# Kernel tuning notes

Hardware: AMD Instinct MI355X
Metric: run time of the kernel (lower is better)

The kernel has to match this reference:

```python
import jax, jax.numpy as jnp
import numpy as np

# dims
B, NB, T, NC = 16, 55, 512, 8          # batch, filter bands, time steps, CSP comps
D, L, H, E, K, F, C = 512, 6, 8, 8, 2, 2048, 2  # embed, depth, heads, experts, top_k, d_ff, classes
DH = D // H
IN = NB * NC  # 440
EPS = 1e-5


def _ln(x, s, b):
    m = x.mean(-1, keepdims=True)
    v = ((x - m) ** 2).mean(-1, keepdims=True)
    return (x - m) / jnp.sqrt(v + EPS) * s + b


def setup_inputs() -> dict:
    key = jax.random.key(0)
    ks = iter(jax.random.split(key, 64))
    n = lambda shape, s=0.02: jax.random.normal(next(ks), shape, jnp.float32) * s
    inp = {
        "x": jax.random.normal(next(ks), (B, NB, T, NC), jnp.float32),
        # frontend
        "proj_w": n((IN, D)), "proj_b": jnp.zeros((D,), jnp.float32),
        "pos": n((1, T, D)),
        "ln_pre_s": jnp.ones((D,), jnp.float32), "ln_pre_b": jnp.zeros((D,), jnp.float32),
        # stacked transformer-block params [L, ...]
        "ln1_s": jnp.ones((L, D), jnp.float32), "ln1_b": jnp.zeros((L, D), jnp.float32),
        "wq": n((L, D, D)), "bq": jnp.zeros((L, D), jnp.float32),
        "wk": n((L, D, D)), "bk": jnp.zeros((L, D), jnp.float32),
        "wv": n((L, D, D)), "bv": jnp.zeros((L, D), jnp.float32),
        "wo": n((L, D, D)), "bo": jnp.zeros((L, D), jnp.float32),
        "ln2_s": jnp.ones((L, D), jnp.float32), "ln2_b": jnp.zeros((L, D), jnp.float32),
        "gate_w": n((L, D, E)),
        "e_w1": n((L, E, D, F)), "e_b1": jnp.zeros((L, E, F), jnp.float32),
        "e_w2": n((L, E, F, D)), "e_b2": jnp.zeros((L, E, D), jnp.float32),
        # classifier head
        "ln_f_s": jnp.ones((D,), jnp.float32), "ln_f_b": jnp.zeros((D,), jnp.float32),
        "head_w": n((D, C)), "head_b": jnp.zeros((C,), jnp.float32),
    }
    return inp


def _moe(h, gw, w1, b1, w2, b2):
    # h: [N, D]; top-K softmax-gated mixture of GELU-FFN experts + load-balance aux loss
    N = h.shape[0]
    probs = jax.nn.softmax(h @ gw, axis=-1)                  # [N, E]
    vals, idx = jax.lax.top_k(probs, K)                      # [N, K]
    w = vals / vals.sum(-1, keepdims=True)                   # renormalized top-k weights
    disp = jax.nn.one_hot(idx, E, dtype=h.dtype)             # [N, K, E]
    combine = (disp * w[..., None]).sum(1)                   # [N, E]
    y = jnp.zeros_like(h)
    for e in range(E):  # small fixed expert loop
        y = y + combine[:, e:e + 1] * (jax.nn.gelu(h @ w1[e] + b1[e]) @ w2[e] + b2[e])
    frac = disp.mean((0, 1)) * K                             # fraction of tokens routed to each expert
    aux = E * jnp.sum(frac * probs.mean(0))
    return y, aux


def reference(x, proj_w, proj_b, pos, ln_pre_s, ln_pre_b, ln1_s, ln1_b, wq, bq, wk, bk,
              wv, bv, wo, bo, ln2_s, ln2_b, gate_w, e_w1, e_b1, e_w2, e_b2,
              ln_f_s, ln_f_b, head_w, head_b):
    b, nb, t, nc = x.shape
    h = x.transpose(0, 2, 1, 3).reshape(b, t, nb * nc) @ proj_w + proj_b  # [B,T,D]
    h = _ln(h + pos[:, :t, :], ln_pre_s, ln_pre_b)
    scale = DH ** -0.5
    total_aux = jnp.float32(0.0)
    for l in range(L):
        # pre-LN multi-head self-attention
        a = _ln(h, ln1_s[l], ln1_b[l])
        q = (a @ wq[l] + bq[l]).reshape(b, t, H, DH)
        k = (a @ wk[l] + bk[l]).reshape(b, t, H, DH)
        v = (a @ wv[l] + bv[l]).reshape(b, t, H, DH)
        att = jax.nn.softmax(jnp.einsum('bqhd,bkhd->bhqk', q, k) * scale, axis=-1)
        o = jnp.einsum('bhqk,bkhd->bqhd', att, v).reshape(b, t, D) @ wo[l] + bo[l]
        h = h + o
        # pre-LN MoE FFN
        m = _ln(h, ln2_s[l], ln2_b[l]).reshape(b * t, D)
        y, aux = _moe(m, gate_w[l], e_w1[l], e_b1[l], e_w2[l], e_b2[l])
        h = h + y.reshape(b, t, D)
        total_aux = total_aux + aux
    pooled = h.mean(axis=1)                                   # [B, D]
    logits = _ln(pooled, ln_f_s, ln_f_b) @ head_w + head_b    # [B, C]
    return logits, total_aux
```

## Files before the change

### kernel.cpp

```cpp
#include <hip/hip_runtime.h>
#include <stdint.h>

typedef unsigned short u16;
typedef unsigned int   u32;
typedef short bh8 __attribute__((ext_vector_type(8)));
typedef float f4  __attribute__((ext_vector_type(4)));

#define NTOK    8192
#define PADROWS 17408
#define MAXTILES 136

__device__ __forceinline__ u16 f2bf(float f){
  u32 u = __float_as_uint(f);
  return (u16)((u + 0x7fffu + ((u>>16)&1u)) >> 16);
}
__device__ __forceinline__ float bf2f(u16 h){ return __uint_as_float(((u32)h)<<16); }
__device__ __forceinline__ u32 pk2(float a, float b){ return (u32)f2bf(a) | ((u32)f2bf(b)<<16); }
__device__ __forceinline__ float gelu_f(float x){
  float u = 0.7978845608028654f*(x + 0.044715f*x*x*x);
  float t = 1.f - 2.f/(__expf(2.f*u)+1.f);
  return 0.5f*x*(1.f+t);
}
__device__ __forceinline__ void gload_lds16(const void* g, void* l){
  __builtin_amdgcn_global_load_lds((const __attribute__((address_space(1))) u32*)g,
                                   (__attribute__((address_space(3))) u32*)l, 16, 0, 0);
}

__global__ __launch_bounds__(256) void xpose_k(const float* __restrict__ x, u16* __restrict__ xt){
  int idx = blockIdx.x*256 + threadIdx.x;
  const float* src = x + (size_t)idx*8;
  float4 a = *(const float4*)src;
  float4 b = *(const float4*)(src+4);
  int t  = idx & 511;
  int nb = (idx>>9) % 55;
  int bb = (idx>>9) / 55;
  uint4 u;
  u.x = pk2(a.x,a.y); u.y = pk2(a.z,a.w); u.z = pk2(b.x,b.y); u.w = pk2(b.z,b.w);
  *(uint4*)&xt[((size_t)(bb*512+t))*448 + nb*8] = u;
}

__device__ __forceinline__ void tile_xpose(const float* __restrict__ src, u16* __restrict__ dst,
                                           int Ksrc, int N, int Kdst, float (*tile)[65])
{
  int tid = threadIdx.x;
  int k0 = blockIdx.y*64, n0 = blockIdx.x*64;
  #pragma unroll
  for (int p=0;p<4;++p){
    int r = p*16 + (tid>>4);
    int c4 = (tid&15)*4;
    int k = k0 + r;
    float4 v = (k < Ksrc) ? *(const float4*)&src[(size_t)k*N + n0 + c4] : (float4){0.f,0.f,0.f,0.f};
    tile[r][c4]=v.x; tile[r][c4+1]=v.y; tile[r][c4+2]=v.z; tile[r][c4+3]=v.w;
  }
  __syncthreads();
  #pragma unroll
  for (int p=0;p<2;++p){
    int rn = p*32 + (tid>>3);
    int ck = (tid&7)*8;
    uint4 u;
    u.x = pk2(tile[ck+0][rn], tile[ck+1][rn]);
    u.y = pk2(tile[ck+2][rn], tile[ck+3][rn]);
    u.z = pk2(tile[ck+4][rn], tile[ck+5][rn]);
    u.w = pk2(tile[ck+6][rn], tile[ck+7][rn]);
    *(uint4*)&dst[(size_t)(n0+rn)*Kdst + k0 + ck] = u;
  }
}

__global__ __launch_bounds__(256) void wconv_k(const float* __restrict__ src, u16* __restrict__ dst,
                                               int Ksrc, int N, int Kdst){
  __shared__ float tile[64][65];
  src += (size_t)blockIdx.z*Ksrc*N;
  dst += (size_t)blockIdx.z*N*Kdst;
  tile_xpose(src, dst, Ksrc, N, Kdst, tile);
}

__global__ __launch_bounds__(256) void wconvqkvo_k(const float* __restrict__ wq, const float* __restrict__ wk,
    const float* __restrict__ wv, const float* __restrict__ wo,
    u16* __restrict__ qkvt, u16* __restrict__ wot)
{
  __shared__ float tile[64][65];
  int z = blockIdx.z;
  int l = z>>2, which = z&3;
  const float* src = ((which==0)? wq : (which==1)? wk : (which==2)? wv : wo) + (size_t)l*512*512;
  u16* dst = (which==3) ? wot + (size_t)l*512*512
                        : qkvt + (size_t)l*1536*512 + (size_t)which*512*512;
  tile_xpose(src, dst, 512, 512, 512, tile);
}

__global__ __launch_bounds__(256) void qkvb_k(const float* __restrict__ bq, const float* __restrict__ bk,
                                              const float* __restrict__ bv, float* __restrict__ qkvb){
  int idx = blockIdx.x*256 + threadIdx.x;
  int l = idx/1536, c = idx - l*1536;
  const float* s = (c<512)? bq : (c<1024)? bk : bv;
  qkvb[idx] = s[l*512 + (c&511)];
}

template<int MODE, bool GATHER>
__global__ __launch_bounds__(256) void gemm2_k(
    const u16* __restrict__ A, int lda,
    const u16* __restrict__ Bt, int ldb, int Ksteps,
    const float* __restrict__ biasBase,
    float* __restrict__ Cf, u16* __restrict__ Cb, int ldc,
    const int* __restrict__ tile_e, const int* __restrict__ toklist,
    const float* __restrict__ wlist, int expN)
{
  __shared__ __align__(16) u16 As[2][128*32];
  __shared__ __align__(16) u16 Bs[2][128*32];
  const int tid = threadIdx.x, lane = tid&63, w = tid>>6;
  const int wr = w>>1, wc = w&1;
  int nx = gridDim.x;
  int nwg = nx * gridDim.y;
  int lin = blockIdx.y*nx + blockIdx.x;
  int qq = nwg>>3, rr = nwg&7, xc = lin&7, oo = lin>>3;
  int wg = (xc<rr ? xc*(qq+1) : rr*(qq+1)+(xc-rr)*qq) + oo;
  int by = wg/nx, bx = wg - by*nx;
  const int n0 = bx*128, m0 = by*128;
  const u16* Bp = Bt;
  const float* bias = biasBase;
  if constexpr (MODE>=3){
    int e = tile_e[by];
    Bp   += (size_t)e*(size_t)expN*(size_t)ldb;
    bias += (size_t)e*(size_t)expN;
  }
  const u16* asrc0; const u16* asrc1; const u16* bsrc0; const u16* bsrc1;
  {
    int idx0 = tid, row0 = idx0>>2, sp0 = idx0&3, ks0 = sp0 ^ ((row0>>1)&3);
    int idx1 = 256+tid, row1 = idx1>>2, sp1 = idx1&3, ks1 = sp1 ^ ((row1>>1)&3);
    size_t ar0 = GATHER ? (size_t)toklist[m0+row0] : (size_t)(m0+row0);
    size_t ar1 = GATHER ? (size_t)toklist[m0+row1] : (size_t)(m0+row1);
    asrc0 = A + ar0*(size_t)lda + ks0*8;
    asrc1 = A + ar1*(size_t)lda + ks1*8;
    bsrc0 = Bp + (size_t)(n0+row0)*ldb + ks0*8;
    bsrc1 = Bp + (size_t)(n0+row1)*ldb + ks1*8;
  }
  f4 acc[4][4];
  #pragma unroll
  for (int i=0;i<4;++i)
    #pragma unroll
    for (int j=0;j<4;++j) acc[i][j] = (f4){0.f,0.f,0.f,0.f};

  gload_lds16(asrc0, &As[0][tid*8]);
  gload_lds16(asrc1, &As[0][(256+tid)*8]);
  gload_lds16(bsrc0, &Bs[0][tid*8]);
  gload_lds16(bsrc1, &Bs[0][(256+tid)*8]);
  asrc0 += 32; asrc1 += 32; bsrc0 += 32; bsrc1 += 32;
  __syncthreads();

  int buf = 0;
  for (int kt=0; kt<Ksteps; ++kt){
    if (kt+1 < Ksteps){
      int nb = buf^1;
      gload_lds16(asrc0, &As[nb][tid*8]);
      gload_lds16(asrc1, &As[nb][(256+tid)*8]);
      gload_lds16(bsrc0, &Bs[nb][tid*8]);
      gload_lds16(bsrc1, &Bs[nb][(256+tid)*8]);
      asrc0 += 32; asrc1 += 32; bsrc0 += 32; bsrc1 += 32;
    }
    bh8 af[4], bf[4];
    const int q = lane>>4;
    #pragma unroll
    for (int mf=0;mf<4;++mf){
      int r = wr*64 + mf*16 + (lane&15);
      af[mf] = *(const bh8*)&As[buf][r*32 + (q ^ ((r>>1)&3))*8];
    }
    #pragma unroll
    for (int nf=0;nf<4;++nf){
      int r = wc*64 + nf*16 + (lane&15);
      bf[nf] = *(const bh8*)&Bs[buf][r*32 + (q ^ ((r>>1)&3))*8];
    }
    #pragma unroll
    for (int mf=0;mf<4;++mf)
      #pragma unroll
      for (int nf=0;nf<4;++nf)
        acc[mf][nf] = __builtin_amdgcn_mfma_f32_16x16x32_bf16(af[mf], bf[nf], acc[mf][nf], 0, 0, 0);
    __syncthreads();
    buf ^= 1;
  }
  #pragma unroll
  for (int mf=0;mf<4;++mf){
    #pragma unroll
    for (int nf=0;nf<4;++nf){
      f4 d = acc[mf][nf];
      int ncol = n0 + wc*64 + nf*16 + (lane&15);
      float bv = bias[ncol];
      #pragma unroll
      for (int r=0;r<4;++r){
        int mrow = m0 + wr*64 + mf*16 + (lane>>4)*4 + r;
        float val = d[r] + bv;
        if constexpr (MODE==0){
          Cf[(size_t)mrow*ldc + ncol] = val;
        } else if constexpr (MODE==1){
          int slab = ncol>>6, dh = ncol&63;
          Cb[((size_t)slab*NTOK + (size_t)mrow)*64 + dh] = f2bf(val);
        } else if constexpr (MODE==2){
          Cf[(size_t)mrow*ldc + ncol] += val;
        } else if constexpr (MODE==3){
          Cb[(size_t)mrow*ldc + ncol] = f2bf(gelu_f(val));
        } else {
          Cb[(size_t)mrow*ldc + ncol] = f2bf(wlist[mrow]*val);
        }
      }
    }
  }
}

template<bool ADDPOS, bool OUTF32>
__global__ __launch_bounds__(256) void ln_k(const float* __restrict__ X, const float* __restrict__ pos,
    const float* __restrict__ sc, const float* __restrict__ bi,
    float* __restrict__ outF, u16* __restrict__ outB)
{
  int tid=threadIdx.x, lane=tid&63, w=tid>>6;
  int row = blockIdx.x*4 + w;
  const float* xr = X + (size_t)row*512 + lane*8;
  float x[8];
  float4 v0 = *(const float4*)xr;
  float4 v1 = *(const float4*)(xr+4);
  x[0]=v0.x;x[1]=v0.y;x[2]=v0.z;x[3]=v0.w;x[4]=v1.x;x[5]=v1.y;x[6]=v1.z;x[7]=v1.w;
  if constexpr (ADDPOS){
    const float* pr = pos + (size_t)(row&511)*512 + lane*8;
    float4 p0 = *(const float4*)pr, p1 = *(const float4*)(pr+4);
    x[0]+=p0.x;x[1]+=p0.y;x[2]+=p0.z;x[3]+=p0.w;x[4]+=p1.x;x[5]+=p1.y;x[6]+=p1.z;x[7]+=p1.w;
  }
  float sm=0.f, sq=0.f;
  #pragma unroll
  for (int i=0;i<8;++i){ sm+=x[i]; sq+=x[i]*x[i]; }
  #pragma unroll
  for (int mk=1; mk<64; mk<<=1){ sm += __shfl_xor(sm, mk); sq += __shfl_xor(sq, mk); }
  float mean = sm*(1.f/512.f);
  float var  = sq*(1.f/512.f) - mean*mean;
  float rstd = rsqrtf(var + 1e-5f);
  int d0 = lane*8;
  float4 s0 = *(const float4*)(sc+d0), s1 = *(const float4*)(sc+d0+4);
  float4 b0 = *(const float4*)(bi+d0), b1 = *(const float4*)(bi+d0+4);
  float y[8];
  y[0]=(x[0]-mean)*rstd*s0.x+b0.x; y[1]=(x[1]-mean)*rstd*s0.y+b0.y;
  y[2]=(x[2]-mean)*rstd*s0.z+b0.z; y[3]=(x[3]-mean)*rstd*s0.w+b0.w;
  y[4]=(x[4]-mean)*rstd*s1.x+b1.x; y[5]=(x[5]-mean)*rstd*s1.y+b1.y;
  y[6]=(x[6]-mean)*rstd*s1.z+b1.z; y[7]=(x[7]-mean)*rstd*s1.w+b1.w;
  if constexpr (OUTF32){
    float4 o0 = {y[0],y[1],y[2],y[3]}, o1 = {y[4],y[5],y[6],y[7]};
    *(float4*)(outF + (size_t)row*512 + d0)     = o0;
    *(float4*)(outF + (size_t)row*512 + d0 + 4) = o1;
  } else {
    uint4 u; u.x=pk2(y[0],y[1]); u.y=pk2(y[2],y[3]); u.z=pk2(y[4],y[5]); u.w=pk2(y[6],y[7]);
    *(uint4*)&outB[(size_t)row*512 + d0] = u;
  }
}

__global__ __launch_bounds__(256) void gatherln_k(float* __restrict__ h,
    const u16* __restrict__ yb, const int* __restrict__ t2pos,
    const float* __restrict__ sc, const float* __restrict__ bi, u16* __restrict__ outB)
{
  int tid=threadIdx.x, lane=tid&63, w=tid>>6;
  int row = blockIdx.x*4 + w;
  float* hp = h + (size_t)row*512 + lane*8;
  float4 v0 = *(float4*)hp, v1 = *(float4*)(hp+4);
  int p0 = t2pos[2*row], p1 = t2pos[2*row+1];
  uint4 ya = *(const uint4*)&yb[(size_t)p0*512 + lane*8];
  uint4 yv = *(const uint4*)&yb[(size_t)p1*512 + lane*8];
  float x[8];
  x[0]=v0.x + bf2f((u16)(ya.x&0xffff)) + bf2f((u16)(yv.x&0xffff));
  x[1]=v0.y + bf2f((u16)(ya.x>>16))    + bf2f((u16)(yv.x>>16));
  x[2]=v0.z + bf2f((u16)(ya.y&0xffff)) + bf2f((u16)(yv.y&0xffff));
  x[3]=v0.w + bf2f((u16)(ya.y>>16))    + bf2f((u16)(yv.y>>16));
  x[4]=v1.x + bf2f((u16)(ya.z&0xffff)) + bf2f((u16)(yv.z&0xffff));
  x[5]=v1.y + bf2f((u16)(ya.z>>16))    + bf2f((u16)(yv.z>>16));
  x[6]=v1.z + bf2f((u16)(ya.w&0xffff)) + bf2f((u16)(yv.w&0xffff));
  x[7]=v1.w + bf2f((u16)(ya.w>>16))    + bf2f((u16)(yv.w>>16));
  float4 o0 = {x[0],x[1],x[2],x[3]}, o1 = {x[4],x[5],x[6],x[7]};
  *(float4*)hp = o0; *(float4*)(hp+4) = o1;
  float sm=0.f, sq=0.f;
  #pragma unroll
  for (int i=0;i<8;++i){ sm+=x[i]; sq+=x[i]*x[i]; }
  #pragma unroll
  for (int mk=1; mk<64; mk<<=1){ sm += __shfl_xor(sm, mk); sq += __shfl_xor(sq, mk); }
  float mean = sm*(1.f/512.f);
  float rstd = rsqrtf(sq*(1.f/512.f) - mean*mean + 1e-5f);
  int d0 = lane*8;
  float4 s0 = *(const float4*)(sc+d0), s1 = *(const float4*)(sc+d0+4);
  float4 b0 = *(const float4*)(bi+d0), b1 = *(const float4*)(bi+d0+4);
  float y[8];
  y[0]=(x[0]-mean)*rstd*s0.x+b0.x; y[1]=(x[1]-mean)*rstd*s0.y+b0.y;
  y[2]=(x[2]-mean)*rstd*s0.z+b0.z; y[3]=(x[3]-mean)*rstd*s0.w+b0.w;
  y[4]=(x[4]-mean)*rstd*s1.x+b1.x; y[5]=(x[5]-mean)*rstd*s1.y+b1.y;
  y[6]=(x[6]-mean)*rstd*s1.z+b1.z; y[7]=(x[7]-mean)*rstd*s1.w+b1.w;
  uint4 u; u.x=pk2(y[0],y[1]); u.y=pk2(y[2],y[3]); u.z=pk2(y[4],y[5]); u.w=pk2(y[6],y[7]);
  *(uint4*)&outB[(size_t)row*512 + d0] = u;
}

__global__ __launch_bounds__(256) void attn_k(const u16* __restrict__ QKV, u16* __restrict__ Og)
{
  __shared__ __align__(16) u16 VT[2][64*72];
  __shared__ __align__(16) u16 PS[4][16*72];
  int tid=threadIdx.x, lane=tid&63, w=tid>>6;
  int qt=blockIdx.x, hh=blockIdx.y, bb=blockIdx.z;
  const u16* Qh = QKV + ((size_t)hh     *NTOK + (size_t)bb*512)*64;
  const u16* Kh = QKV + ((size_t)(8+hh) *NTOK + (size_t)bb*512)*64;
  const u16* Vh = QKV + ((size_t)(16+hh)*NTOK + (size_t)bb*512)*64;
  size_t obase = (size_t)bb*512*512 + (size_t)hh*64;
  int qrow0 = qt*64 + w*16;
  bh8 qf[2];
  #pragma unroll
  for (int kf=0;kf<2;++kf)
    qf[kf] = *(const bh8*)&Qh[ (size_t)(qrow0 + (lane&15))*64 + kf*32 + (lane>>4)*8 ];
  f4 oacc[4];
  #pragma unroll
  for (int i=0;i<4;++i) oacc[i] = (f4){0.f,0.f,0.f,0.f};
  float mrun[4] = {-1e30f,-1e30f,-1e30f,-1e30f};
  float lrun[4] = {0.f,0.f,0.f,0.f};
  const float scale = 0.125f;

  for (int kt=0; kt<8; ++kt){
    const int buf = kt&1;
    #pragma unroll
    for (int r2=0;r2<2;++r2){
      int idx = r2*256 + tid;
      int dhg = idx&7;
      int dh0 = dhg*8, key = idx>>3;
      uint4 raw = *(const uint4*)&Vh[ (size_t)(kt*64+key)*64 + dh0 ];
      int kx = key ^ (dhg<<3);
      u32 rw[4] = {raw.x, raw.y, raw.z, raw.w};
      #pragma unroll
      for (int j=0;j<4;++j){
        VT[buf][(dh0+2*j  )*72 + kx] = (u16)(rw[j]&0xffff);
        VT[buf][(dh0+2*j+1)*72 + kx] = (u16)(rw[j]>>16);
      }
    }
    f4 s[4];
    #pragma unroll
    for (int nf=0;nf<4;++nf){
      size_t krow = (size_t)(kt*64+nf*16+(lane&15))*64 + (lane>>4)*8;
      bh8 k0 = *(const bh8*)&Kh[krow];
      bh8 k1 = *(const bh8*)&Kh[krow+32];
      f4 z = (f4){0.f,0.f,0.f,0.f};
      z = __builtin_amdgcn_mfma_f32_16x16x32_bf16(qf[0], k0, z, 0,0,0);
      z = __builtin_amdgcn_mfma_f32_16x16x32_bf16(qf[1], k1, z, 0,0,0);
      s[nf] = z;
    }
    float pe[4][4];
    #pragma unroll
    for (int r=0;r<4;++r){
      float sv0=s[0][r]*scale, sv1=s[1][r]*scale, sv2=s[2][r]*scale, sv3=s[3][r]*scale;
      float mt = fmaxf(fmaxf(sv0,sv1), fmaxf(sv2,sv3));
      #pragma unroll
      for (int mk=1; mk<16; mk<<=1) mt = fmaxf(mt, __shfl_xor(mt, mk));
      float mn = fmaxf(mrun[r], mt);
      float sf = __expf(mrun[r]-mn);
      float p0=__expf(sv0-mn), p1=__expf(sv1-mn), p2=__expf(sv2-mn), p3=__expf(sv3-mn);
      pe[0][r]=p0; pe[1][r]=p1; pe[2][r]=p2; pe[3][r]=p3;
      float rs = p0+p1+p2+p3;
      #pragma unroll
      for (int mk=1; mk<16; mk<<=1) rs += __shfl_xor(rs, mk);
      lrun[r] = lrun[r]*sf + rs;
      mrun[r] = mn;
      #pragma unroll
      for (int df=0;df<4;++df) oacc[df][r] *= sf;
    }
    #pragma unroll
    for (int nf=0;nf<4;++nf)
      #pragma unroll
      for (int r=0;r<4;++r)
        PS[w][ ((lane>>4)*4+r)*72 + nf*16 + (lane&15) ] = f2bf(pe[nf][r]);
    __syncthreads();
    #pragma unroll
    for (int ks=0;ks<2;++ks){
      bh8 pa = *(const bh8*)&PS[w][ (lane&15)*72 + ks*32 + (lane>>4)*8 ];
      #pragma unroll
      for (int df=0;df<4;++df){
        int dh = df*16 + (lane&15);
        int sgrp = (dh>>3)&7;
        bh8 vb = *(const bh8*)&VT[buf][ dh*72 + ((ks*4 + (lane>>4)) ^ sgrp)*8 ];
        oacc[df] = __builtin_amdgcn_mfma_f32_16x16x32_bf16(pa, vb, oacc[df], 0,0,0);
      }
    }
  }
  #pragma unroll
  for (int df=0;df<4;++df)
    #pragma unroll
    for (int r=0;r<4;++r){
      int qr = qrow0 + (lane>>4)*4 + r;
      float ov = oacc[df][r] / lrun[r];
      Og[ obase + (size_t)qr*512 + df*16 + (lane&15) ] = f2bf(ov);
    }
}

__global__ __launch_bounds__(256) void lnroute_k(const float* __restrict__ h,
    const float* __restrict__ sc, const float* __restrict__ bi, u16* __restrict__ outB,
    const float* __restrict__ gw,
    float* __restrict__ psum, int* __restrict__ cnt, int* __restrict__ t2e, float* __restrict__ t2w)
{
  __shared__ float ps[8]; __shared__ int cs[8];
  int tid=threadIdx.x, lane=tid&63, w=tid>>6;
  if (tid<8){ ps[tid]=0.f; cs[tid]=0; }
  __syncthreads();
  int d0 = lane*8;
  float4 s0 = *(const float4*)(sc+d0), s1 = *(const float4*)(sc+d0+4);
  float4 b0 = *(const float4*)(bi+d0), b1 = *(const float4*)(bi+d0+4);
  for (int it=0; it<4; ++it){
    int t = blockIdx.x*16 + w*4 + it;
    const float* xr = h + (size_t)t*512 + d0;
    float x[8];
    float4 v0 = *(const float4*)xr, v1 = *(const float4*)(xr+4);
    x[0]=v0.x;x[1]=v0.y;x[2]=v0.z;x[3]=v0.w;x[4]=v1.x;x[5]=v1.y;x[6]=v1.z;x[7]=v1.w;
    float sm=0.f, sq=0.f;
    #pragma unroll
    for (int i=0;i<8;++i){ sm+=x[i]; sq+=x[i]*x[i]; }
    #pragma unroll
    for (int mk=1; mk<64; mk<<=1){ sm += __shfl_xor(sm, mk); sq += __shfl_xor(sq, mk); }
    float mean = sm*(1.f/512.f);
    float rstd = rsqrtf(sq*(1.f/512.f) - mean*mean + 1e-5f);
    float y[8];
    y[0]=(x[0]-mean)*rstd*s0.x+b0.x; y[1]=(x[1]-mean)*rstd*s0.y+b0.y;
    y[2]=(x[2]-mean)*rstd*s0.z+b0.z; y[3]=(x[3]-mean)*rstd*s0.w+b0.w;
    y[4]=(x[4]-mean)*rstd*s1.x+b1.x; y[5]=(x[5]-mean)*rstd*s1.y+b1.y;
    y[6]=(x[6]-mean)*rstd*s1.z+b1.z; y[7]=(x[7]-mean)*rstd*s1.w+b1.w;
    uint4 u; u.x=pk2(y[0],y[1]); u.y=pk2(y[2],y[3]); u.z=pk2(y[4],y[5]); u.w=pk2(y[6],y[7]);
    *(uint4*)&outB[(size_t)t*512 + d0] = u;
    float acc[8] = {0,0,0,0,0,0,0,0};
    #pragma unroll
    for (int j=0;j<8;++j){
      const float* g = gw + (size_t)(d0+j)*8;
      float4 g0 = *(const float4*)g, g1 = *(const float4*)(g+4);
      acc[0]+=y[j]*g0.x; acc[1]+=y[j]*g0.y; acc[2]+=y[j]*g0.z; acc[3]+=y[j]*g0.w;
      acc[4]+=y[j]*g1.x; acc[5]+=y[j]*g1.y; acc[6]+=y[j]*g1.z; acc[7]+=y[j]*g1.w;
    }
    #pragma unroll
    for (int mk=1; mk<64; mk<<=1)
      #pragma unroll
      for (int e=0;e<8;++e) acc[e] += __shfl_xor(acc[e], mk);
    if (lane==0){
      float mx=acc[0];
      #pragma unroll
      for (int e=1;e<8;++e) mx = fmaxf(mx, acc[e]);
      float pe[8], tot=0.f;
      #pragma unroll
      for (int e=0;e<8;++e){ pe[e]=__expf(acc[e]-mx); tot+=pe[e]; }
      float inv = 1.f/tot;
      #pragma unroll
      for (int e=0;e<8;++e) pe[e]*=inv;
      int e0=0; float v0=pe[0];
      #pragma unroll
      for (int e=1;e<8;++e) if (pe[e]>v0){ v0=pe[e]; e0=e; }
      int e1=-1; float v1=-1.f;
      #pragma unroll
      for (int e=0;e<8;++e) if (e!=e0 && pe[e]>v1){ v1=pe[e]; e1=e; }
      float invw = 1.f/(v0+v1);
      t2e[2*t]=e0; t2w[2*t]=v0*invw; t2e[2*t+1]=e1; t2w[2*t+1]=v1*invw;
      #pragma unroll
      for (int e=0;e<8;++e) atomicAdd(&ps[e], pe[e]);
      atomicAdd(&cs[e0],1); atomicAdd(&cs[e1],1);
    }
  }
  __syncthreads();
  if (tid<8){ atomicAdd(&psum[tid], ps[tid]); atomicAdd(&cnt[tid], cs[tid]); }
}

__global__ __launch_bounds__(256) void offsets_k(const int* __restrict__ cnt, const float* __restrict__ psum,
    int* __restrict__ offs, int* __restrict__ fill, int* __restrict__ tile_e,
    int* __restrict__ toklist, float* __restrict__ wlist, float* __restrict__ auxp)
{
  int tid = threadIdx.x, b = blockIdx.x;
  int i = b*256 + tid;
  if (i < PADROWS){ toklist[i]=0; wlist[i]=0.f; }
  if (b==0){
    if (tid==0){
      int off=0; float auxl=0.f;
      for (int e=0;e<8;++e){
        offs[e] = off;
        int reg = (cnt[e]+127)&~127;
        int t0 = off>>7, t1 = (off+reg)>>7;
        for (int t=t0;t<t1;++t) tile_e[t]=e;
        off += reg;
        auxl += ((float)cnt[e]*(1.f/8192.f)) * (psum[e]*(1.f/8192.f));
      }
      for (int t=off>>7; t<MAXTILES; ++t) tile_e[t]=0;
      auxp[0] += 8.f*auxl;
    }
    if (tid<8) fill[tid]=0;
  }
}

__global__ __launch_bounds__(256) void scatter_k(const int* __restrict__ t2e, const float* __restrict__ t2w,
    const int* __restrict__ offs, int* __restrict__ fill,
    int* __restrict__ toklist, float* __restrict__ wlist, int* __restrict__ t2pos)
{
  int t = blockIdx.x*256 + threadIdx.x;
  #pragma unroll
  for (int kk=0;kk<2;++kk){
    int e = t2e[2*t+kk];
    int p = atomicAdd(&fill[e], 1);
    int i = offs[e] + p;
    toklist[i] = t; wlist[i] = t2w[2*t+kk]; t2pos[2*t+kk] = i;
  }
}

__global__ __launch_bounds__(256) void gather_k(float* __restrict__ h, const u16* __restrict__ yb,
                                                const int* __restrict__ t2pos)
{
  int tid = threadIdx.x;
  int t = blockIdx.x*4 + (tid>>6);
  int lane = tid&63;
  int p0 = t2pos[2*t], p1 = t2pos[2*t+1];
  uint4 a = *(const uint4*)&yb[(size_t)p0*512 + lane*8];
  uint4 b = *(const uint4*)&yb[(size_t)p1*512 + lane*8];
  float* hp = h + (size_t)t*512 + lane*8;
  float4 h0 = *(float4*)hp, h1 = *(float4*)(hp+4);
  h0.x += bf2f((u16)(a.x&0xffff)) + bf2f((u16)(b.x&0xffff));
  h0.y += bf2f((u16)(a.x>>16))    + bf2f((u16)(b.x>>16));
  h0.z += bf2f((u16)(a.y&0xffff)) + bf2f((u16)(b.y&0xffff));
  h0.w += bf2f((u16)(a.y>>16))    + bf2f((u16)(b.y>>16));
  h1.x += bf2f((u16)(a.z&0xffff)) + bf2f((u16)(b.z&0xffff));
  h1.y += bf2f((u16)(a.z>>16))    + bf2f((u16)(b.z>>16));
  h1.z += bf2f((u16)(a.w&0xffff)) + bf2f((u16)(b.w&0xffff));
  h1.w += bf2f((u16)(a.w>>16))    + bf2f((u16)(b.w>>16));
  *(float4*)hp = h0; *(float4*)(hp+4) = h1;
}

__global__ __launch_bounds__(256) void pool_k(const float* __restrict__ h, float* __restrict__ pooled){
  int idx = blockIdx.x*256 + threadIdx.x;
  int bb = idx>>9, d = idx&511;
  const float* p = h + (size_t)bb*512*512 + d;
  float s=0.f;
  for (int t=0;t<512;++t) s += p[(size_t)t*512];
  pooled[idx] = s*(1.f/512.f);
}

__global__ __launch_bounds__(256) void head_k(const float* __restrict__ pooled,
    const float* __restrict__ sc, const float* __restrict__ bi,
    const float* __restrict__ hw, const float* __restrict__ hb,
    const float* __restrict__ auxp, float* __restrict__ out)
{
  int tid=threadIdx.x, lane=tid&63, w=tid>>6;
  for (int i=0;i<4;++i){
    int row = w*4+i;
    const float* xr = pooled + (size_t)row*512 + lane*8;
    float x[8];
    float4 v0 = *(const float4*)xr, v1 = *(const float4*)(xr+4);
    x[0]=v0.x;x[1]=v0.y;x[2]=v0.z;x[3]=v0.w;x[4]=v1.x;x[5]=v1.y;x[6]=v1.z;x[7]=v1.w;
    float sm=0.f, sq=0.f;
    #pragma unroll
    for (int j=0;j<8;++j){ sm+=x[j]; sq+=x[j]*x[j]; }
    #pragma unroll
    for (int mk=1; mk<64; mk<<=1){ sm += __shfl_xor(sm, mk); sq += __shfl_xor(sq, mk); }
    float mean = sm*(1.f/512.f);
    float rstd = rsqrtf(sq*(1.f/512.f) - mean*mean + 1e-5f);
    int d0 = lane*8;
    float c0=0.f, c1=0.f;
    #pragma unroll
    for (int j=0;j<8;++j){
      float yv = (x[j]-mean)*rstd*sc[d0+j] + bi[d0+j];
      c0 += yv*hw[(d0+j)*2]; c1 += yv*hw[(d0+j)*2+1];
    }
    #pragma unroll
    for (int mk=1; mk<64; mk<<=1){ c0 += __shfl_xor(c0, mk); c1 += __shfl_xor(c1, mk); }
    if (lane==0){ out[row*2+0] = c0 + hb[0]; out[row*2+1] = c1 + hb[1]; }
  }
  if (tid==0) out[32] = auxp[0];
}

extern "C" void kernel_launch(void* const* d_in, const int* in_sizes, int n_in,
                              void* d_out, int out_size, void* d_ws, size_t ws_size,
                              hipStream_t stream)
{
  (void)in_sizes; (void)n_in; (void)out_size; (void)ws_size;
  const float* x      = (const float*)d_in[0];
  const float* proj_w = (const float*)d_in[1];
  const float* proj_b = (const float*)d_in[2];
  const float* pos    = (const float*)d_in[3];
  const float* ln_pre_s=(const float*)d_in[4];
  const float* ln_pre_b=(const float*)d_in[5];
  const float* ln1_s  = (const float*)d_in[6];
  const float* ln1_b  = (const float*)d_in[7];
  const float* wq     = (const float*)d_in[8];
  const float* bq     = (const float*)d_in[9];
  const float* wk     = (const float*)d_in[10];
  const float* bk     = (const float*)d_in[11];
  const float* wv     = (const float*)d_in[12];
  const float* bv     = (const float*)d_in[13];
  const float* wo     = (const float*)d_in[14];
  const float* bo     = (const float*)d_in[15];
  const float* ln2_s  = (const float*)d_in[16];
  const float* ln2_b  = (const float*)d_in[17];
  const float* gate_w = (const float*)d_in[18];
  const float* e_w1   = (const float*)d_in[19];
  const float* e_b1   = (const float*)d_in[20];
  const float* e_w2   = (const float*)d_in[21];
  const float* e_b2   = (const float*)d_in[22];
  const float* ln_f_s = (const float*)d_in[23];
  const float* ln_f_b = (const float*)d_in[24];
  const float* head_w = (const float*)d_in[25];
  const float* head_b = (const float*)d_in[26];

  char* base = (char*)d_ws;
  size_t off = 0;
  auto carve = [&](size_t bytes)->char*{
    char* r = base + off; off += (bytes + 255) & ~(size_t)255; return r;
  };
  u16*   xt      = (u16*)  carve((size_t)8192*448*2);
  float* h       = (float*)carve((size_t)8192*512*4);
  u16*   a       = (u16*)  carve((size_t)8192*512*2);
  u16*   qkv     = (u16*)  carve((size_t)8192*1536*2);
  u16*   ob      = (u16*)  carve((size_t)8192*512*2);
  u16*   hidden  = (u16*)  carve((size_t)PADROWS*2048*2);
  u16*   ybuf    = (u16*)  carve((size_t)PADROWS*512*2);
  u16*   projt   = (u16*)  carve((size_t)512*448*2);
  u16*   qkvt    = (u16*)  carve((size_t)6*1536*512*2);
  u16*   wot     = (u16*)  carve((size_t)6*512*512*2);
  u16*   w1t     = (u16*)  carve((size_t)6*8*2048*512*2);
  u16*   w2t     = (u16*)  carve((size_t)6*8*512*2048*2);
  float* qkvb    = (float*)carve((size_t)6*1536*4);
  int*   toklist = (int*)  carve(PADROWS*4);
  float* wlist   = (float*)carve(PADROWS*4);
  int*   tile_e  = (int*)  carve(256*4);
  int*   rcntA   = (int*)  carve(6*16*4);
  int*   fill    = (int*)  carve(64);
  int*   offs    = (int*)  carve(64);
  int*   t2e     = (int*)  carve(16384*4);
  float* t2w     = (float*)carve(16384*4);
  int*   t2pos   = (int*)  carve(16384*4);
  float* pooled  = (float*)carve(8192*4);
  float* auxp    = (float*)carve(256);

  hipMemsetAsync(xt, 0, (size_t)8192*448*2, stream);
  hipMemsetAsync(rcntA, 0, 6*16*4, stream);
  hipMemsetAsync(auxp, 0, 4, stream);

  xpose_k<<<1760, 256, 0, stream>>>(x, xt);
  wconv_k<<<dim3(8,7,1), 256, 0, stream>>>(proj_w, projt, 440, 512, 448);
  wconvqkvo_k<<<dim3(8,8,24), 256, 0, stream>>>(wq, wk, wv, wo, qkvt, wot);
  wconv_k<<<dim3(32,8,48), 256, 0, stream>>>(e_w1, w1t, 512, 2048, 512);
  wconv_k<<<dim3(8,32,48), 256, 0, stream>>>(e_w2, w2t, 2048, 512, 2048);
  qkvb_k<<<36, 256, 0, stream>>>(bq, bk, bv, qkvb);
  gemm2_k<0,false><<<dim3(4,64), 256, 0, stream>>>(xt, 448, projt, 448, 14, proj_b,
      h, nullptr, 512, nullptr, nullptr, nullptr, 0);
  ln_k<true,true><<<2048, 256, 0, stream>>>(h, pos, ln_pre_s, ln_pre_b, h, nullptr);

  for (int l=0; l<6; ++l){
    int*   cnt  = rcntA + l*16;
    float* psum = (float*)(cnt + 8);
    if (l == 0)
      ln_k<false,false><<<2048, 256, 0, stream>>>(h, nullptr, ln1_s, ln1_b, nullptr, a);
    else
      gatherln_k<<<2048, 256, 0, stream>>>(h, ybuf, t2pos,
          ln1_s+(size_t)l*512, ln1_b+(size_t)l*512, a);
    gemm2_k<1,false><<<dim3(12,64), 256, 0, stream>>>(a, 512, qkvt+(size_t)l*1536*512, 512, 16,
        qkvb+(size_t)l*1536, nullptr, qkv, 1536, nullptr, nullptr, nullptr, 0);
    attn_k<<<dim3(8,8,16), 256, 0, stream>>>(qkv, ob);
    gemm2_k<2,false><<<dim3(4,64), 256, 0, stream>>>(ob, 512, wot+(size_t)l*512*512, 512, 16,
        bo+(size_t)l*512, h, nullptr, 512, nullptr, nullptr, nullptr, 0);
    lnroute_k<<<512, 256, 0, stream>>>(h, ln2_s+(size_t)l*512, ln2_b+(size_t)l*512, a,
        gate_w+(size_t)l*512*8, psum, cnt, t2e, t2w);
    offsets_k<<<68, 256, 0, stream>>>(cnt, psum, offs, fill, tile_e, toklist, wlist, auxp);
    scatter_k<<<32, 256, 0, stream>>>(t2e, t2w, offs, fill, toklist, wlist, t2pos);
    gemm2_k<3,true ><<<dim3(16,MAXTILES), 256, 0, stream>>>(a, 512, w1t+(size_t)l*8*2048*512, 512, 16,
        e_b1 + (size_t)l*8*2048, nullptr, hidden, 2048, tile_e, toklist, wlist, 2048);
    gemm2_k<4,false><<<dim3(4,MAXTILES), 256, 0, stream>>>(hidden, 2048, w2t+(size_t)l*8*512*2048, 2048, 64,
        e_b2 + (size_t)l*8*512, nullptr, ybuf, 512, tile_e, nullptr, wlist, 512);
  }

  gather_k<<<2048, 256, 0, stream>>>(h, ybuf, t2pos);
  pool_k<<<32, 256, 0, stream>>>(h, pooled);
  head_k<<<1, 256, 0, stream>>>(pooled, ln_f_s, ln_f_b, head_w, head_b, auxp, (float*)d_out);
}
```

Before: 2.322 ms.

## Store V transposed in QKV GEMM epilogue and read it directly in attention

The QKV projection epilogue now writes the V slabs in a dh-major (transposed) layout as packed bf16 pairs, while Q and K keep the old layout. The attention kernel drops its per-tile LDS transpose of V and the block-wide barrier, and loads the MFMA B-operand fragments for V straight from global memory. This removes the LDS shuffle and the synchronisation from the attention loop. In exchange the GEMM epilogue does strided scattered stores, and attention relies on cache hits for repeated V reads.

```diff
diff --git a/kernel.cpp b/kernel.cpp
--- a/kernel.cpp
+++ b/kernel.cpp
@@ -183,21 +183,33 @@
       f4 d = acc[mf][nf];
       int ncol = n0 + wc*64 + nf*16 + (lane&15);
       float bv = bias[ncol];
-      #pragma unroll
-      for (int r=0;r<4;++r){
-        int mrow = m0 + wr*64 + mf*16 + (lane>>4)*4 + r;
-        float val = d[r] + bv;
-        if constexpr (MODE==0){
-          Cf[(size_t)mrow*ldc + ncol] = val;
-        } else if constexpr (MODE==1){
-          int slab = ncol>>6, dh = ncol&63;
-          Cb[((size_t)slab*NTOK + (size_t)mrow)*64 + dh] = f2bf(val);
-        } else if constexpr (MODE==2){
-          Cf[(size_t)mrow*ldc + ncol] += val;
-        } else if constexpr (MODE==3){
-          Cb[(size_t)mrow*ldc + ncol] = f2bf(gelu_f(val));
+      int mrow0 = m0 + wr*64 + mf*16 + (lane>>4)*4;
+      if constexpr (MODE==1){
+        int slab = ncol>>6, dh = ncol&63;
+        if (slab < 16){
+          #pragma unroll
+          for (int r=0;r<4;++r)
+            Cb[((size_t)slab*NTOK + (size_t)(mrow0+r))*64 + dh] = f2bf(d[r]+bv);
         } else {
-          Cb[(size_t)mrow*ldc + ncol] = f2bf(wlist[mrow]*val);
+          uint2 u;
+          u.x = pk2(d[0]+bv, d[1]+bv);
+          u.y = pk2(d[2]+bv, d[3]+bv);
+          *(uint2*)&Cb[(size_t)slab*NTOK*64 + (size_t)dh*NTOK + mrow0] = u;
+        }
+      } else {
+        #pragma unroll
+        for (int r=0;r<4;++r){
+          int mrow = mrow0 + r;
+          float val = d[r] + bv;
+          if constexpr (MODE==0){
+            Cf[(size_t)mrow*ldc + ncol] = val;
+          } else if constexpr (MODE==2){
+            Cf[(size_t)mrow*ldc + ncol] += val;
+          } else if constexpr (MODE==3){
+            Cb[(size_t)mrow*ldc + ncol] = f2bf(gelu_f(val));
+          } else {
+            Cb[(size_t)mrow*ldc + ncol] = f2bf(wlist[mrow]*val);
+          }
         }
       }
     }
@@ -290,13 +302,12 @@
 
 __global__ __launch_bounds__(256) void attn_k(const u16* __restrict__ QKV, u16* __restrict__ Og)
 {
-  __shared__ __align__(16) u16 VT[2][64*72];
   __shared__ __align__(16) u16 PS[4][16*72];
   int tid=threadIdx.x, lane=tid&63, w=tid>>6;
   int qt=blockIdx.x, hh=blockIdx.y, bb=blockIdx.z;
   const u16* Qh = QKV + ((size_t)hh     *NTOK + (size_t)bb*512)*64;
   const u16* Kh = QKV + ((size_t)(8+hh) *NTOK + (size_t)bb*512)*64;
-  const u16* Vh = QKV + ((size_t)(16+hh)*NTOK + (size_t)bb*512)*64;
+  const u16* Vt = QKV + (size_t)(16+hh)*NTOK*64 + (size_t)bb*512;
   size_t obase = (size_t)bb*512*512 + (size_t)hh*64;
   int qrow0 = qt*64 + w*16;
   bh8 qf[2];
@@ -311,21 +322,6 @@
   const float scale = 0.125f;
 
   for (int kt=0; kt<8; ++kt){
-    const int buf = kt&1;
-    #pragma unroll
-    for (int r2=0;r2<2;++r2){
-      int idx = r2*256 + tid;
-      int dhg = idx&7;
-      int dh0 = dhg*8, key = idx>>3;
-      uint4 raw = *(const uint4*)&Vh[ (size_t)(kt*64+key)*64 + dh0 ];
-      int kx = key ^ (dhg<<3);
-      u32 rw[4] = {raw.x, raw.y, raw.z, raw.w};
-      #pragma unroll
-      for (int j=0;j<4;++j){
-        VT[buf][(dh0+2*j  )*72 + kx] = (u16)(rw[j]&0xffff);
-        VT[buf][(dh0+2*j+1)*72 + kx] = (u16)(rw[j]>>16);
-      }
-    }
     f4 s[4];
     #pragma unroll
     for (int nf=0;nf<4;++nf){
@@ -361,15 +357,13 @@
       #pragma unroll
       for (int r=0;r<4;++r)
         PS[w][ ((lane>>4)*4+r)*72 + nf*16 + (lane&15) ] = f2bf(pe[nf][r]);
-    __syncthreads();
     #pragma unroll
     for (int ks=0;ks<2;++ks){
       bh8 pa = *(const bh8*)&PS[w][ (lane&15)*72 + ks*32 + (lane>>4)*8 ];
       #pragma unroll
       for (int df=0;df<4;++df){
-        int dh = df*16 + (lane&15);
-        int sgrp = (dh>>3)&7;
-        bh8 vb = *(const bh8*)&VT[buf][ dh*72 + ((ks*4 + (lane>>4)) ^ sgrp)*8 ];
+        const u16* vp = &Vt[ (size_t)(df*16+(lane&15))*NTOK + kt*64 + ks*32 + (lane>>4)*8 ];
+        bh8 vb = *(const bh8*)vp;
         oacc[df] = __builtin_amdgcn_mfma_f32_16x16x32_bf16(pa, vb, oacc[df], 0,0,0);
       }
     }
```

New measurement: 2.444 ms. 1.05x slower.

## Prefetch V tiles into registers and pack key pairs in attention LDS

Applied to the files above, without the earlier changes.

Restructures the attention kernel's V staging. The next V tile is loaded into registers while the current tile's QK^T and softmax run, then written as packed key-pair u32 words into an LDS buffer with an odd (33-word) row stride, leaving one barrier per iteration instead of a load-then-barrier sequence. It also raises wave priority around the MFMA sections. The risk is that the 16-byte LDS reads at the odd stride may be misaligned and split into slower accesses; the lnroute edits only rename variables.

```diff
diff --git a/kernel.cpp b/kernel.cpp
--- a/kernel.cpp
+++ b/kernel.cpp
@@ -290,7 +290,7 @@
 
 __global__ __launch_bounds__(256) void attn_k(const u16* __restrict__ QKV, u16* __restrict__ Og)
 {
-  __shared__ __align__(16) u16 VT[2][64*72];
+  __shared__ __align__(16) u32 VT[2][64*33];
   __shared__ __align__(16) u16 PS[4][16*72];
   int tid=threadIdx.x, lane=tid&63, w=tid>>6;
   int qt=blockIdx.x, hh=blockIdx.y, bb=blockIdx.z;
@@ -310,23 +310,31 @@
   float lrun[4] = {0.f,0.f,0.f,0.f};
   const float scale = 0.125f;
 
+  const int dhg = tid&7, kp = tid>>3, dh0 = dhg*8;
+  const u16* vbase = Vh + (size_t)(2*kp)*64 + dh0;
+  uint4 va, vb2;
+
+  va  = *(const uint4*)vbase;
+  vb2 = *(const uint4*)(vbase + 64);
+  {
+    u32 aw[4] = {va.x,va.y,va.z,va.w}, bw[4] = {vb2.x,vb2.y,vb2.z,vb2.w};
+    #pragma unroll
+    for (int j2=0;j2<4;++j2){
+      VT[0][(dh0+2*j2  )*33 + kp] = (aw[j2]&0xffffu) | (bw[j2]<<16);
+      VT[0][(dh0+2*j2+1)*33 + kp] = (aw[j2]>>16)     | (bw[j2]&0xffff0000u);
+    }
+  }
+
   for (int kt=0; kt<8; ++kt){
     const int buf = kt&1;
-    #pragma unroll
-    for (int r2=0;r2<2;++r2){
-      int idx = r2*256 + tid;
-      int dhg = idx&7;
-      int dh0 = dhg*8, key = idx>>3;
-      uint4 raw = *(const uint4*)&Vh[ (size_t)(kt*64+key)*64 + dh0 ];
-      int kx = key ^ (dhg<<3);
-      u32 rw[4] = {raw.x, raw.y, raw.z, raw.w};
-      #pragma unroll
-      for (int j=0;j<4;++j){
-        VT[buf][(dh0+2*j  )*72 + kx] = (u16)(rw[j]&0xffff);
-        VT[buf][(dh0+2*j+1)*72 + kx] = (u16)(rw[j]>>16);
-      }
-    }
-    f4 s[4];
+    __syncthreads();
+    if (kt < 7){
+      const u16* s = vbase + (size_t)(kt+1)*64*64;
+      va  = *(const uint4*)s;
+      vb2 = *(const uint4*)(s + 64);
+    }
+    f4 s4[4];
+    __builtin_amdgcn_s_setprio(1);
     #pragma unroll
     for (int nf=0;nf<4;++nf){
       size_t krow = (size_t)(kt*64+nf*16+(lane&15))*64 + (lane>>4)*8;
@@ -335,12 +343,13 @@
       f4 z = (f4){0.f,0.f,0.f,0.f};
       z = __builtin_amdgcn_mfma_f32_16x16x32_bf16(qf[0], k0, z, 0,0,0);
       z = __builtin_amdgcn_mfma_f32_16x16x32_bf16(qf[1], k1, z, 0,0,0);
-      s[nf] = z;
-    }
+      s4[nf] = z;
+    }
+    __builtin_amdgcn_s_setprio(0);
     float pe[4][4];
     #pragma unroll
     for (int r=0;r<4;++r){
-      float sv0=s[0][r]*scale, sv1=s[1][r]*scale, sv2=s[2][r]*scale, sv3=s[3][r]*scale;
+      float sv0=s4[0][r]*scale, sv1=s4[1][r]*scale, sv2=s4[2][r]*scale, sv3=s4[3][r]*scale;
       float mt = fmaxf(fmaxf(sv0,sv1), fmaxf(sv2,sv3));
       #pragma unroll
       for (int mk=1; mk<16; mk<<=1) mt = fmaxf(mt, __shfl_xor(mt, mk));
@@ -361,18 +370,27 @@
       #pragma unroll
       for (int r=0;r<4;++r)
         PS[w][ ((lane>>4)*4+r)*72 + nf*16 + (lane&15) ] = f2bf(pe[nf][r]);
-    __syncthreads();
+    if (kt < 7){
+      u32 aw[4] = {va.x,va.y,va.z,va.w}, bw[4] = {vb2.x,vb2.y,vb2.z,vb2.w};
+      #pragma unroll
+      for (int j2=0;j2<4;++j2){
+        VT[buf^1][(dh0+2*j2  )*33 + kp] = (aw[j2]&0xffffu) | (bw[j2]<<16);
+        VT[buf^1][(dh0+2*j2+1)*33 + kp] = (aw[j2]>>16)     | (bw[j2]&0xffff0000u);
+      }
+    }
+    __builtin_amdgcn_s_setprio(1);
     #pragma unroll
     for (int ks=0;ks<2;++ks){
       bh8 pa = *(const bh8*)&PS[w][ (lane&15)*72 + ks*32 + (lane>>4)*8 ];
       #pragma unroll
       for (int df=0;df<4;++df){
         int dh = df*16 + (lane&15);
-        int sgrp = (dh>>3)&7;
-        bh8 vb = *(const bh8*)&VT[buf][ dh*72 + ((ks*4 + (lane>>4)) ^ sgrp)*8 ];
-        oacc[df] = __builtin_amdgcn_mfma_f32_16x16x32_bf16(pa, vb, oacc[df], 0,0,0);
+        const u32* vp = &VT[buf][ dh*33 + ks*16 + (lane>>4)*4 ];
+        bh8 vv = *(const bh8*)vp;
+        oacc[df] = __builtin_amdgcn_mfma_f32_16x16x32_bf16(pa, vv, oacc[df], 0,0,0);
       }
     }
+    __builtin_amdgcn_s_setprio(0);
   }
   #pragma unroll
   for (int df=0;df<4;++df)
@@ -438,14 +456,14 @@
       float inv = 1.f/tot;
       #pragma unroll
       for (int e=0;e<8;++e) pe[e]*=inv;
-      int e0=0; float v0=pe[0];
-      #pragma unroll
-      for (int e=1;e<8;++e) if (pe[e]>v0){ v0=pe[e]; e0=e; }
-      int e1=-1; float v1=-1.f;
-      #pragma unroll
-      for (int e=0;e<8;++e) if (e!=e0 && pe[e]>v1){ v1=pe[e]; e1=e; }
-      float invw = 1.f/(v0+v1);
-      t2e[2*t]=e0; t2w[2*t]=v0*invw; t2e[2*t+1]=e1; t2w[2*t+1]=v1*invw;
+      int e0=0; float v0e=pe[0];
+      #pragma unroll
+      for (int e=1;e<8;++e) if (pe[e]>v0e){ v0e=pe[e]; e0=e; }
+      int e1=-1; float v1e=-1.f;
+      #pragma unroll
+      for (int e=0;e<8;++e) if (e!=e0 && pe[e]>v1e){ v1e=pe[e]; e1=e; }
+      float invw = 1.f/(v0e+v1e);
+      t2e[2*t]=e0; t2w[2*t]=v0e*invw; t2e[2*t+1]=e1; t2w[2*t+1]=v1e*invw;
       #pragma unroll
       for (int e=0;e<8;++e) atomicAdd(&ps[e], pe[e]);
       atomicAdd(&cs[e0],1); atomicAdd(&cs[e1],1);
```

Measured after the change: 2.433 ms. 1.05x slower.
